# Optimization experiments

Hardware: AMD Instinct MI355X
Metric: run time of the kernel (lower is better)

Reference implementation:

```python
import jax, jax.numpy as jnp
import numpy as np

N, D, H, C, E = 16384, 768, 768, 2, 20

def setup_inputs() -> dict:
    key = jax.random.key(0)
    k1, k2, k3, k4, k5, k6 = jax.random.split(key, 6)
    return {
        "embeddings": jax.random.normal(k1, (N, D), dtype=jnp.float32),
        "component_idx": jax.random.randint(k2, (N,), 0, E, dtype=jnp.int64),
        "W1": jax.random.normal(k3, (E, D, H), dtype=jnp.float32) * (1.0 / np.sqrt(D)),
        "b1": jnp.zeros((E, H), dtype=jnp.float32),
        "W2": jax.random.normal(k4, (E, H, C), dtype=jnp.float32) * (1.0 / np.sqrt(H)),
        "b2": jnp.zeros((E, C), dtype=jnp.float32),
    }

def reference(embeddings, component_idx, W1, b1, W2, b2):
    # Each token n goes through expert component_idx[n]:
    #   y = relu(x @ W1[e] + b1[e]) @ W2[e] + b2[e]
    # The torch module's mask/cat/argsort reassembly is mathematically a
    # per-token select of its own expert's output at the original position.
    # Dense-expert formulation (standard jax MoE fallback), then gather.
    h = jax.nn.relu(jnp.einsum('nd,edh->enh', embeddings, W1) + b1[:, None, :])  # [E,N,H]
    y = jnp.einsum('enh,ehc->enc', h, W2) + b2[:, None, :]                        # [E,N,C]
    n_idx = jnp.arange(embeddings.shape[0])
    return y[component_idx, n_idx]  # [N,C]
```

## Files before the change

### kernel.cpp

```cpp
#include <hip/hip_runtime.h>

#define N_D 768
#define N_H 768
#define N_C 2
#define N_E 20
#define MT 128
#define NT 128
#define BK 32
#define KT (N_D / BK)
#define MAX_TILES 160
#define ROWB (N_D * 2)

typedef __attribute__((ext_vector_type(8))) short short8;
typedef __attribute__((ext_vector_type(4))) float f32x4;

__device__ __forceinline__ unsigned short f2bf(float f) {
  unsigned u = __builtin_bit_cast(unsigned, f);
  u += 0x7FFFu + ((u >> 16) & 1u);
  return (unsigned short)(u >> 16);
}

#define GLD_LDS16(gp, lp)                                                        \
  __builtin_amdgcn_global_load_lds(                                              \
      (const __attribute__((address_space(1))) void*)(gp),                       \
      (__attribute__((address_space(3))) void*)(lp), 16, 0, 0)


__global__ __launch_bounds__(256) void k_hist(const int* __restrict__ cidx,
                                              int* __restrict__ counts, int n) {
  __shared__ int lc[N_E];
  if (threadIdx.x < N_E) lc[threadIdx.x] = 0;
  __syncthreads();
  for (int i = blockIdx.x * blockDim.x + threadIdx.x; i < n;
       i += gridDim.x * blockDim.x) {
    int e = cidx[i];
    e = e < 0 ? 0 : (e >= N_E ? N_E - 1 : e);
    atomicAdd(&lc[e], 1);
  }
  __syncthreads();
  if (threadIdx.x < N_E) atomicAdd(&counts[threadIdx.x], lc[threadIdx.x]);
}

__global__ void k_scan(const int* __restrict__ counts, int* __restrict__ offsets,
                       int* __restrict__ cursor, int* __restrict__ tiles,
                       int* __restrict__ numTiles) {
  if (threadIdx.x == 0) {
    int run = 0, t = 0;
    for (int e = 0; e < N_E; ++e) {
      offsets[e] = run;
      cursor[e] = run;
      int nt = (counts[e] + MT - 1) / MT;
      for (int m = 0; m < nt && t < MAX_TILES; ++m) tiles[t++] = (e << 8) | m;
      run += counts[e];
    }
    *numTiles = t;
  }
}

__global__ __launch_bounds__(256) void k_scatter(const int* __restrict__ cidx,
                                                 int* __restrict__ cursor,
                                                 int* __restrict__ sorted, int n) {
  __shared__ int lc[N_E];
  __shared__ int lbase[N_E];
  int tid = threadIdx.x;
  if (tid < N_E) lc[tid] = 0;
  __syncthreads();
  int i = blockIdx.x * blockDim.x + tid;
  int e = 0, p = 0;
  if (i < n) {
    e = cidx[i];
    e = e < 0 ? 0 : (e >= N_E ? N_E - 1 : e);
    p = atomicAdd(&lc[e], 1);
  }
  __syncthreads();
  if (tid < N_E) lbase[tid] = atomicAdd(&cursor[tid], lc[tid]);
  __syncthreads();
  if (i < n) sorted[lbase[e] + p] = i;
}


__global__ __launch_bounds__(192) void k_gather(const float* __restrict__ emb,
                                                const int* __restrict__ sorted,
                                                unsigned short* __restrict__ Xg,
                                                int n) {
  int row = blockIdx.x;
  int j = threadIdx.x;
  ushort4 o;
  if (row < n) {
    float4 v = ((const float4*)(emb + (size_t)sorted[row] * N_D))[j];
    o.x = f2bf(v.x);
    o.y = f2bf(v.y);
    o.z = f2bf(v.z);
    o.w = f2bf(v.w);
  } else {
    o.x = o.y = o.z = o.w = 0;
  }
  ((ushort4*)(Xg + (size_t)row * N_D))[j] = o;
}


__global__ __launch_bounds__(256) void k_w1_cvt(const float* __restrict__ W1,
                                                unsigned short* __restrict__ W1t) {
  __shared__ float tile[64][65];
  int e = blockIdx.z, h0 = blockIdx.x * 64, d0 = blockIdx.y * 64;
  const float* src = W1 + (size_t)e * N_D * N_H;
  unsigned short* dst = W1t + (size_t)e * N_H * N_D;
  int tx = threadIdx.x & 15, ty = threadIdx.x >> 4;
  for (int s = 0; s < 4; ++s) {
    int d = s * 16 + ty;
    float4 v = *(const float4*)&src[(size_t)(d0 + d) * N_H + h0 + tx * 4];
    tile[d][tx * 4 + 0] = v.x;
    tile[d][tx * 4 + 1] = v.y;
    tile[d][tx * 4 + 2] = v.z;
    tile[d][tx * 4 + 3] = v.w;
  }
  __syncthreads();
  int px = threadIdx.x & 7, py = threadIdx.x >> 3;
  for (int s = 0; s < 2; ++s) {
    int h = s * 32 + py;
    short8 v;
    for (int j = 0; j < 8; ++j)
      v[j] = (short)f2bf(tile[px * 8 + j][h]);
    *(short8*)&dst[(size_t)(h0 + h) * N_D + d0 + px * 8] = v;
  }
}


__global__ __launch_bounds__(256, 2) void k_gemm(
    const unsigned short* __restrict__ Xg, const unsigned short* __restrict__ W1t,
    const float* __restrict__ b1, const float* __restrict__ W2,
    const float* __restrict__ b2, const int* __restrict__ sorted,
    const int* __restrict__ counts, const int* __restrict__ offsets,
    const int* __restrict__ tiles, const int* __restrict__ numTiles,
    float* __restrict__ out) {
  if ((int)blockIdx.y >= *numTiles) return;
  const int tv = tiles[blockIdx.y];
  const int e = tv >> 8;
  const int m0 = (tv & 255) * MT;
  const int off = offsets[e];
  const int cnt_rel = counts[e] - m0;
  const int n0 = blockIdx.x * NT;

  __shared__ unsigned short lA[2][MT * BK];
  __shared__ unsigned short lB[2][NT * BK];

  const int tid = threadIdx.x;
  const int wid = tid >> 6, lane = tid & 63;
  const int wm = (wid >> 1) * 64, wn = (wid & 1) * 64;
  const int quad = lane >> 4, lm = lane & 15;

  const int R0 = wid * 32 + lm;
  const char* agp = (const char*)Xg + (size_t)(off + m0 + R0) * ROWB + quad * 16;
  const char* bgp = (const char*)W1t + (size_t)e * N_H * ROWB +
                    (size_t)(n0 + R0) * ROWB + quad * 16;
  unsigned short* lap[2] = {&lA[0][(wid * 32) * BK], &lA[1][(wid * 32) * BK]};
  unsigned short* lbp[2] = {&lB[0][(wid * 32) * BK], &lB[1][(wid * 32) * BK]};

#define ISSUE_BATCH(kk, b)                                                       \
  do {                                                                           \
    const char* a_ = agp + (kk)*64;                                              \
    const char* b_ = bgp + (kk)*64;                                              \
    GLD_LDS16(a_, lap[b]);                                                       \
    GLD_LDS16(a_ + 16 * ROWB, lap[b] + 16 * BK);                                 \
    GLD_LDS16(b_, lbp[b]);                                                       \
    GLD_LDS16(b_ + 16 * ROWB, lbp[b] + 16 * BK);                                 \
  } while (0)

  f32x4 acc[4][4] = {};

  ISSUE_BATCH(0, 0);
  ISSUE_BATCH(1, 1);

  const int fa = quad * 128 + lm * 8;

  for (int kt = 0; kt < KT; ++kt) {
    const int cur = kt & 1;
    asm volatile("s_waitcnt vmcnt(4)\n\ts_barrier" ::: "memory");
    short8 af[4], bfr[4];
    for (int i = 0; i < 4; ++i)
      af[i] = *(const short8*)&lA[cur][((wm >> 4) + i) * 512 + fa];
    for (int j = 0; j < 4; ++j)
      bfr[j] = *(const short8*)&lB[cur][((wn >> 4) + j) * 512 + fa];
    asm volatile("s_waitcnt lgkmcnt(0)\n\ts_barrier" ::: "memory");
    int kk = kt + 2;
    if (kk >= KT) kk -= KT;
    ISSUE_BATCH(kk, cur);
    for (int i = 0; i < 4; ++i)
      for (int j = 0; j < 4; ++j)
        acc[i][j] =
            __builtin_amdgcn_mfma_f32_16x16x32_bf16(af[i], bfr[j], acc[i][j], 0, 0, 0);
  }

  float y0[4][4], y1[4][4];
  for (int i = 0; i < 4; ++i)
    for (int r = 0; r < 4; ++r) y0[i][r] = y1[i][r] = 0.f;

  for (int j = 0; j < 4; ++j) {
    int col = n0 + wn + j * 16 + lm;
    float bias = b1[e * N_H + col];
    float2 w2 = *(const float2*)&W2[((size_t)e * N_H + col) * N_C];
    for (int i = 0; i < 4; ++i) {
      f32x4 a = acc[i][j];
      for (int r = 0; r < 4; ++r) {
        float h = a[r] + bias;
        h = h > 0.f ? h : 0.f;
        y0[i][r] += h * w2.x;
        y1[i][r] += h * w2.y;
      }
    }
  }
  for (int s = 1; s < 16; s <<= 1) {
    for (int i = 0; i < 4; ++i)
      for (int r = 0; r < 4; ++r) {
        y0[i][r] += __shfl_xor(y0[i][r], s, 64);
        y1[i][r] += __shfl_xor(y1[i][r], s, 64);
      }
  }
  if (lm == 0) {
    const bool add_bias = (n0 == 0) && (wn == 0);
    float bb0 = add_bias ? b2[e * N_C + 0] : 0.f;
    float bb1 = add_bias ? b2[e * N_C + 1] : 0.f;
    for (int i = 0; i < 4; ++i) {
      for (int r = 0; r < 4; ++r) {
        int mrel = wm + i * 16 + quad * 4 + r;
        if (mrel < cnt_rel) {
          int token = sorted[off + m0 + mrel];
          atomicAdd(&out[(size_t)token * N_C + 0], y0[i][r] + bb0);
          atomicAdd(&out[(size_t)token * N_C + 1], y1[i][r] + bb1);
        }
      }
    }
  }
}


extern "C" void kernel_launch(void* const* d_in, const int* in_sizes, int n_in,
                              void* d_out, int out_size, void* d_ws, size_t ws_size,
                              hipStream_t stream) {
  const float* emb = (const float*)d_in[0];
  const int* cidx = (const int*)d_in[1];
  const float* W1 = (const float*)d_in[2];
  const float* b1 = (const float*)d_in[3];
  const float* W2 = (const float*)d_in[4];
  const float* b2 = (const float*)d_in[5];
  float* out = (float*)d_out;
  const int n = in_sizes[1];

  char* ws = (char*)d_ws;
  int* counts = (int*)ws;
  int* offsets = (int*)(ws + 128);
  int* cursor = (int*)(ws + 256);
  int* numTiles = (int*)(ws + 384);
  int* tiles = (int*)(ws + 512);
  int* sorted = (int*)(ws + 2048);
  size_t sorted_bytes = ((size_t)n * 4 + 255) & ~(size_t)255;
  unsigned short* Xg = (unsigned short*)(ws + 2048 + sorted_bytes);
  int pcap = n + MT;
  unsigned short* W1t = Xg + (size_t)pcap * N_D;

  hipMemsetAsync(d_ws, 0, 2048, stream);
  hipMemsetAsync(d_out, 0, (size_t)out_size * sizeof(float), stream);
  int nb = (n + 255) / 256;
  k_hist<<<nb, 256, 0, stream>>>(cidx, counts, n);
  k_scan<<<1, 64, 0, stream>>>(counts, offsets, cursor, tiles, numTiles);
  k_scatter<<<nb, 256, 0, stream>>>(cidx, cursor, sorted, n);
  k_gather<<<pcap, 192, 0, stream>>>(emb, sorted, Xg, n);
  k_w1_cvt<<<dim3(N_H / 64, N_D / 64, N_E), 256, 0, stream>>>(W1, W1t);
  k_gemm<<<dim3(N_H / NT, MAX_TILES), 256, 0, stream>>>(
      Xg, W1t, b1, W2, b2, sorted, counts, offsets, tiles, numTiles, out);
}
```

Measured before the change: 225.6 us.

## Fuse scatter with bf16 gather and remap GEMM workgroups across XCDs

Scatter and gather now run as one kernel. Each block handles 64 tokens, computes their sorted positions, and writes those rows to their sorted slots as bf16, reading the embeddings contiguously in token order. This removes a kernel launch and the dependent read of the sorted index array. An extra block zero-fills the padding rows. The GEMM maps linear block IDs so that consecutive workgroups sharing a tile land on the same XCD, which should improve L2 reuse of the A tile. It also drops work on inactive tiles earlier. The remap assumes 8 XCDs with round-robin dispatch.

```diff
diff --git a/kernel.cpp b/kernel.cpp
--- a/kernel.cpp
+++ b/kernel.cpp
@@ -9,6 +9,7 @@
 #define BK 32
 #define KT (N_D / BK)
 #define MAX_TILES 160
+#define NCOL (N_H / NT)
 #define ROWB (N_D * 2)
 
 typedef __attribute__((ext_vector_type(8))) short short8;
@@ -57,17 +58,30 @@
   }
 }
 
-__global__ __launch_bounds__(256) void k_scatter(const int* __restrict__ cidx,
-                                                 int* __restrict__ cursor,
-                                                 int* __restrict__ sorted, int n) {
+
+#define SG_TOK 64
+
+__global__ __launch_bounds__(256) void k_scatter_gather(
+    const int* __restrict__ cidx, int* __restrict__ cursor,
+    int* __restrict__ sorted, const float* __restrict__ emb,
+    unsigned short* __restrict__ Xg, int n) {
   __shared__ int lc[N_E];
   __shared__ int lbase[N_E];
-  int tid = threadIdx.x;
+  __shared__ int pos_s[SG_TOK];
+  const int tid = threadIdx.x;
+  const int nb = (n + SG_TOK - 1) / SG_TOK;
+  if ((int)blockIdx.x >= nb) {
+    ushort4 z = {0, 0, 0, 0};
+    ushort4* dst = (ushort4*)(Xg + (size_t)n * N_D);
+    for (int k = tid; k < MT * N_D / 4; k += 256) dst[k] = z;
+    return;
+  }
+  const int base_tok = blockIdx.x * SG_TOK;
   if (tid < N_E) lc[tid] = 0;
   __syncthreads();
-  int i = blockIdx.x * blockDim.x + tid;
+  const int i = base_tok + tid;
   int e = 0, p = 0;
-  if (i < n) {
+  if (tid < SG_TOK && i < n) {
     e = cidx[i];
     e = e < 0 ? 0 : (e >= N_E ? N_E - 1 : e);
     p = atomicAdd(&lc[e], 1);
@@ -75,27 +89,33 @@
   __syncthreads();
   if (tid < N_E) lbase[tid] = atomicAdd(&cursor[tid], lc[tid]);
   __syncthreads();
-  if (i < n) sorted[lbase[e] + p] = i;
-}
-
-
-__global__ __launch_bounds__(192) void k_gather(const float* __restrict__ emb,
-                                                const int* __restrict__ sorted,
-                                                unsigned short* __restrict__ Xg,
-                                                int n) {
-  int row = blockIdx.x;
-  int j = threadIdx.x;
-  ushort4 o;
-  if (row < n) {
-    float4 v = ((const float4*)(emb + (size_t)sorted[row] * N_D))[j];
-    o.x = f2bf(v.x);
-    o.y = f2bf(v.y);
-    o.z = f2bf(v.z);
-    o.w = f2bf(v.w);
-  } else {
-    o.x = o.y = o.z = o.w = 0;
-  }
-  ((ushort4*)(Xg + (size_t)row * N_D))[j] = o;
+  if (tid < SG_TOK) {
+    if (i < n) {
+      int pos = lbase[e] + p;
+      sorted[pos] = i;
+      pos_s[tid] = pos;
+    } else {
+      pos_s[tid] = -1;
+    }
+  }
+  __syncthreads();
+  const int wid = tid >> 6, lane = tid & 63;
+  int nrows = n - base_tok;
+  if (nrows > SG_TOK) nrows = SG_TOK;
+  for (int rr = wid; rr < nrows; rr += 4) {
+    const float4* s = (const float4*)(emb + (size_t)(base_tok + rr) * N_D);
+    ushort4* d = (ushort4*)(Xg + (size_t)pos_s[rr] * N_D);
+#pragma unroll
+    for (int p2 = 0; p2 < 3; ++p2) {
+      float4 v = s[lane + p2 * 64];
+      ushort4 o;
+      o.x = f2bf(v.x);
+      o.y = f2bf(v.y);
+      o.z = f2bf(v.z);
+      o.w = f2bf(v.w);
+      d[lane + p2 * 64] = o;
+    }
+  }
 }
 
 
@@ -133,13 +153,20 @@
     const int* __restrict__ counts, const int* __restrict__ offsets,
     const int* __restrict__ tiles, const int* __restrict__ numTiles,
     float* __restrict__ out) {
-  if ((int)blockIdx.y >= *numTiles) return;
-  const int tv = tiles[blockIdx.y];
+  const int nactive = *numTiles * NCOL;
+  const int lin = (int)blockIdx.y * NCOL + (int)blockIdx.x;
+  if (lin >= nactive) return;
+  const int q = nactive >> 3, r = nactive & 7;
+  const int c = lin & 7, ii = lin >> 3;
+  const int wgid = (c < r ? c * (q + 1) : r * (q + 1) + (c - r) * q) + ii;
+  const int tileIdx = wgid / NCOL;
+  const int n0 = (wgid - tileIdx * NCOL) * NT;
+
+  const int tv = tiles[tileIdx];
   const int e = tv >> 8;
   const int m0 = (tv & 255) * MT;
   const int off = offsets[e];
   const int cnt_rel = counts[e] - m0;
-  const int n0 = blockIdx.x * NT;
 
   __shared__ unsigned short lA[2][MT * BK];
   __shared__ unsigned short lB[2][NT * BK];
@@ -193,7 +220,7 @@
 
   float y0[4][4], y1[4][4];
   for (int i = 0; i < 4; ++i)
-    for (int r = 0; r < 4; ++r) y0[i][r] = y1[i][r] = 0.f;
+    for (int r2 = 0; r2 < 4; ++r2) y0[i][r2] = y1[i][r2] = 0.f;
 
   for (int j = 0; j < 4; ++j) {
     int col = n0 + wn + j * 16 + lm;
@@ -201,19 +228,19 @@
     float2 w2 = *(const float2*)&W2[((size_t)e * N_H + col) * N_C];
     for (int i = 0; i < 4; ++i) {
       f32x4 a = acc[i][j];
-      for (int r = 0; r < 4; ++r) {
-        float h = a[r] + bias;
+      for (int r2 = 0; r2 < 4; ++r2) {
+        float h = a[r2] + bias;
         h = h > 0.f ? h : 0.f;
-        y0[i][r] += h * w2.x;
-        y1[i][r] += h * w2.y;
+        y0[i][r2] += h * w2.x;
+        y1[i][r2] += h * w2.y;
       }
     }
   }
   for (int s = 1; s < 16; s <<= 1) {
     for (int i = 0; i < 4; ++i)
-      for (int r = 0; r < 4; ++r) {
-        y0[i][r] += __shfl_xor(y0[i][r], s, 64);
-        y1[i][r] += __shfl_xor(y1[i][r], s, 64);
+      for (int r2 = 0; r2 < 4; ++r2) {
+        y0[i][r2] += __shfl_xor(y0[i][r2], s, 64);
+        y1[i][r2] += __shfl_xor(y1[i][r2], s, 64);
       }
   }
   if (lm == 0) {
@@ -221,12 +248,12 @@
     float bb0 = add_bias ? b2[e * N_C + 0] : 0.f;
     float bb1 = add_bias ? b2[e * N_C + 1] : 0.f;
     for (int i = 0; i < 4; ++i) {
-      for (int r = 0; r < 4; ++r) {
-        int mrel = wm + i * 16 + quad * 4 + r;
+      for (int r2 = 0; r2 < 4; ++r2) {
+        int mrel = wm + i * 16 + quad * 4 + r2;
         if (mrel < cnt_rel) {
           int token = sorted[off + m0 + mrel];
-          atomicAdd(&out[(size_t)token * N_C + 0], y0[i][r] + bb0);
-          atomicAdd(&out[(size_t)token * N_C + 1], y1[i][r] + bb1);
+          atomicAdd(&out[(size_t)token * N_C + 0], y0[i][r2] + bb0);
+          atomicAdd(&out[(size_t)token * N_C + 1], y1[i][r2] + bb1);
         }
       }
     }
@@ -263,9 +290,9 @@
   int nb = (n + 255) / 256;
   k_hist<<<nb, 256, 0, stream>>>(cidx, counts, n);
   k_scan<<<1, 64, 0, stream>>>(counts, offsets, cursor, tiles, numTiles);
-  k_scatter<<<nb, 256, 0, stream>>>(cidx, cursor, sorted, n);
-  k_gather<<<pcap, 192, 0, stream>>>(emb, sorted, Xg, n);
+  int nb64 = (n + SG_TOK - 1) / SG_TOK;
+  k_scatter_gather<<<nb64 + 1, 256, 0, stream>>>(cidx, cursor, sorted, emb, Xg, n);
   k_w1_cvt<<<dim3(N_H / 64, N_D / 64, N_E), 256, 0, stream>>>(W1, W1t);
-  k_gemm<<<dim3(N_H / NT, MAX_TILES), 256, 0, stream>>>(
+  k_gemm<<<dim3(NCOL, MAX_TILES), 256, 0, stream>>>(
       Xg, W1t, b1, W2, b2, sorted, counts, offsets, tiles, numTiles, out);
 }
```

Measured after the change: 221.3 us. No clear change (-1.9%).
